# Kernel tuning notes

Hardware: AMD Instinct MI355X
Metric: run time of the kernel (lower is better)

Reference implementation:

```python
import jax, jax.numpy as jnp
import numpy as np

N_NODES = 100000
N_EDGES = 1600000
IN_DIM = 33
HID = 128
N_CLASSES = 10
N_GRAPHS = 128


def _glorot(key, shape):
    fan_in, fan_out = shape[0], shape[1]
    lim = (6.0 / (fan_in + fan_out)) ** 0.5
    return jax.random.uniform(key, shape, jnp.float32, -lim, lim)


def setup_inputs() -> dict:
    key = jax.random.key(0)
    ks = jax.random.split(key, 20)
    x = jax.random.normal(ks[0], (N_NODES, IN_DIM), jnp.float32)
    edge_index = jax.random.randint(ks[1], (2, N_EDGES), 0, N_NODES, jnp.int64)
    edge_w = jax.random.uniform(ks[2], (N_EDGES,), jnp.float32)
    batch = jnp.sort(jax.random.randint(ks[3], (N_NODES,), 0, N_GRAPHS, jnp.int64))
    p = {
        "We": _glorot(ks[4], (IN_DIM, HID)), "be": jnp.zeros((HID,), jnp.float32),
        "W1": _glorot(ks[5], (HID, HID)), "b1": jnp.zeros((HID,), jnp.float32),
        "W2": _glorot(ks[6], (HID, HID)), "b2": jnp.zeros((HID,), jnp.float32),
        "W3": _glorot(ks[7], (HID, HID)), "b3": jnp.zeros((HID,), jnp.float32),
        "W4": _glorot(ks[8], (HID, HID)), "b4": jnp.zeros((HID,), jnp.float32),
        "Wr1": _glorot(ks[9], (HID, HID // 2)), "br1": jnp.zeros((HID // 2,), jnp.float32),
        "Wr2": _glorot(ks[10], (HID // 2, HID // 4)), "br2": jnp.zeros((HID // 4,), jnp.float32),
        "Wr3": _glorot(ks[11], (HID // 4, N_CLASSES)),
    }
    return dict(x=x, edge_index=edge_index, edge_w=edge_w, batch=batch, **p)


def reference(x, edge_index, edge_w, batch,
              We, be, W1, b1, W2, b2, W3, b3, W4, b4,
              Wr1, br1, Wr2, br2, Wr3):
    N = x.shape[0]
    row, col = edge_index[0], edge_index[1]
    # PyG gcn_norm with add_self_loops=True: append (i,i) edges with weight 1
    loop = jnp.arange(N)
    row2 = jnp.concatenate([row, loop])
    col2 = jnp.concatenate([col, loop])
    w2 = jnp.concatenate([edge_w, jnp.ones((N,), edge_w.dtype)])
    deg = jax.ops.segment_sum(w2, col2, num_segments=N)  # in-degree incl. self-loop
    dinv = jnp.where(deg > 0, deg ** -0.5, 0.0)
    norm = dinv[row2] * w2 * dinv[col2]  # [E+N] symmetric normalization

    def conv(h, W, b):
        h = h @ W  # linear transform first (PyG GCNConv)
        msg = norm[:, None] * h[row2]  # gather + scale
        return jax.ops.segment_sum(msg, col2, num_segments=N) + b  # scatter-add to targets

    h = x @ We + be
    h = jax.nn.relu(conv(h, W1, b1))
    h = jax.nn.relu(conv(h, W2, b2))
    h = jax.nn.relu(conv(h, W3, b3))
    h = jax.nn.relu(conv(h, W4, b4))

    # global mean pool over graphs
    sums = jax.ops.segment_sum(h, batch, num_segments=N_GRAPHS)
    cnt = jax.ops.segment_sum(jnp.ones((N,), h.dtype), batch, num_segments=N_GRAPHS)
    pooled = sums / jnp.maximum(cnt, 1.0)[:, None]  # [G, HID]

    r = jax.nn.relu(pooled @ Wr1 + br1)
    r = jax.nn.relu(r @ Wr2 + br2)
    return r @ Wr3  # [G, n_classes]
```

## Files before the change

kernel.cpp:

```cpp
#include <hip/hip_runtime.h>
#include <hip/hip_bf16.h>

#define NN 100000
#define NE 1600000
#define IN_DIM 33
#define HID 128
#define NG 128
#define NCLS 10

using short8 = __attribute__((ext_vector_type(8))) short;
using floatx4 = __attribute__((ext_vector_type(4))) float;

static __device__ __forceinline__ size_t szmul(int a, int b) {
    return (size_t)a * (size_t)b;
}

static __device__ __forceinline__ unsigned short f2bf(float f) {
    unsigned u = __float_as_uint(f);
    u += 0x7fffu + ((u >> 16) & 1u);
    return (unsigned short)(u >> 16);
}
static __device__ __forceinline__ float bf_lo(unsigned u) { return __uint_as_float(u << 16); }
static __device__ __forceinline__ float bf_hi(unsigned u) { return __uint_as_float(u & 0xffff0000u); }

__global__ void k_init(int* bucket_cnt, int* bucket_fill, float* gsum) {
    int i = blockIdx.x * blockDim.x + threadIdx.x;
    if (i < 513) { bucket_cnt[i] = 0; bucket_fill[i] = 0; }
    if (i < NG * HID) gsum[i] = 0.0f;
}


__global__ __launch_bounds__(256) void k_bhist(const int* __restrict__ col,
                                               int* __restrict__ bucket_cnt, int e, int nbk) {
    __shared__ int hist[512];
    int tid = threadIdx.x;
    for (int i = tid; i < nbk; i += 256) hist[i] = 0;
    __syncthreads();
    for (int i = blockIdx.x * 256 + tid; i < e; i += 256 * 256)
        atomicAdd(&hist[col[i] >> 8], 1);
    __syncthreads();
    for (int i = tid; i < nbk; i += 256)
        if (hist[i]) atomicAdd(&bucket_cnt[i], hist[i]);
}

__global__ void k_scan_small(int* data, int nb) {
    __shared__ int s[512];
    int t = threadIdx.x;
    int v = (t < nb) ? data[t] : 0;
    s[t] = v;
    __syncthreads();
    for (int o = 1; o < 512; o <<= 1) {
        int a = (t >= o) ? s[t - o] : 0;
        __syncthreads();
        s[t] += a;
        __syncthreads();
    }
    if (t < nb) data[t] = s[t] - v;
    if (t == nb - 1) data[nb] = s[t];
}

__global__ __launch_bounds__(256) void k_bin_scatter(const int* __restrict__ row,
                                                     const int* __restrict__ col,
                                                     const float* __restrict__ w,
                                                     const int* __restrict__ bucket_base,
                                                     int* __restrict__ bucket_fill,
                                                     uint2* __restrict__ binned, int e, int nbk) {
    __shared__ int hist[512], rnk[512], basub[512];
    int tid = threadIdx.x;
    int c0 = blockIdx.x * 4096;
    for (int i = tid; i < nbk; i += 256) { hist[i] = 0; rnk[i] = 0; }
    __syncthreads();
    int myb[16]; unsigned myp[16]; unsigned myw[16];
#pragma unroll
    for (int u = 0; u < 16; ++u) {
        int idx = c0 + u * 256 + tid;
        int b = -1;
        if (idx < e) {
            int c = col[idx];
            int r = row[idx];
            myw[u] = __float_as_uint(w[idx]);
            b = c >> 8;
            myp[u] = ((unsigned)(c & 255) << 17) | (unsigned)r;
            atomicAdd(&hist[b], 1);
        }
        myb[u] = b;
    }
    __syncthreads();
    for (int i = tid; i < nbk; i += 256) {
        int c = hist[i];
        basub[i] = (c > 0) ? (bucket_base[i] + atomicAdd(&bucket_fill[i], c)) : 0;
    }
    __syncthreads();
#pragma unroll
    for (int u = 0; u < 16; ++u) {
        int b = myb[u];
        if (b >= 0) {
            int rk = atomicAdd(&rnk[b], 1);
            binned[basub[b] + rk] = make_uint2(myp[u], myw[u]);
        }
    }
}

__global__ __launch_bounds__(256) void k_bucket_cnt(const uint2* __restrict__ binned,
                                                    const int* __restrict__ bucket_base,
                                                    int* __restrict__ cnt,
                                                    float* __restrict__ wsum, int n) {
    __shared__ int c256[256];
    __shared__ float s256[256];
    int b = blockIdx.x, tid = threadIdx.x;
    c256[tid] = 0;
    s256[tid] = 0.0f;
    __syncthreads();
    int beg = bucket_base[b], end = bucket_base[b + 1];
    for (int e2 = beg + tid; e2 < end; e2 += 256) {
        uint2 rec = binned[e2];
        int lo = (rec.x >> 17) & 255;
        atomicAdd(&c256[lo], 1);
        atomicAdd(&s256[lo], __uint_as_float(rec.y));
    }
    __syncthreads();
    int node = b * 256 + tid;
    if (node < n) { cnt[node] = c256[tid]; wsum[node] = s256[tid]; }
}

__global__ void k_dinv(float* __restrict__ dinv, float* __restrict__ selfn, int n) {
    int i = blockIdx.x * blockDim.x + threadIdx.x;
    if (i >= n) return;
    float d = 1.0f + dinv[i];
    float di = (d > 0.0f) ? (1.0f / sqrtf(d)) : 0.0f;
    dinv[i] = di;
    selfn[i] = di * di;
}

#define SCAN_B 1024
__global__ void k_scan1(const int* __restrict__ cnt, int* __restrict__ rowptr,
                        int* __restrict__ bsums, int n) {
    __shared__ int s[SCAN_B];
    int t = threadIdx.x;
    int i = blockIdx.x * SCAN_B + t;
    int v = (i < n) ? cnt[i] : 0;
    s[t] = v;
    __syncthreads();
    for (int o = 1; o < SCAN_B; o <<= 1) {
        int a = (t >= o) ? s[t - o] : 0;
        __syncthreads();
        s[t] += a;
        __syncthreads();
    }
    if (i < n) rowptr[i] = s[t] - v;
    if (t == SCAN_B - 1) bsums[blockIdx.x] = s[t];
}

__global__ void k_scan3(int* rowptr, const int* __restrict__ bsums, int n, int etot) {
    int i = blockIdx.x * blockDim.x + threadIdx.x;
    if (i < n) rowptr[i] += bsums[i >> 10];
    else if (i == n) rowptr[n] = etot;
}

__global__ __launch_bounds__(256) void k_bucket_scatter(const uint2* __restrict__ binned,
                                                        const int* __restrict__ bucket_base,
                                                        const int* __restrict__ rowptr,
                                                        const float* __restrict__ dinv,
                                                        int2* __restrict__ csr, int n) {
    __shared__ int f256[256];
    int b = blockIdx.x, tid = threadIdx.x;
    f256[tid] = 0;
    __syncthreads();
    int beg = bucket_base[b], end = bucket_base[b + 1];
    for (int e2 = beg + tid; e2 < end; e2 += 256) {
        uint2 rec = binned[e2];
        int lo = (rec.x >> 17) & 255;
        int node = (b << 8) | lo;
        int src = rec.x & 0x1FFFF;
        float nw = dinv[src] * __uint_as_float(rec.y) * dinv[node];
        int pos = rowptr[node] + atomicAdd(&f256[lo], 1);
        csr[pos] = make_int2(src, __float_as_int(nw));
    }
    (void)n;
}

__global__ void k_combine(const float* __restrict__ We, const float* __restrict__ W1,
                          const float* __restrict__ be,
                          float* __restrict__ M, float* __restrict__ v) {
    int f = threadIdx.x;
    int k = blockIdx.x;
    if (k < IN_DIM) {
        float a = 0.0f;
#pragma unroll 8
        for (int j = 0; j < HID; ++j) a += We[k * HID + j] * W1[j * HID + f];
        M[k * HID + f] = a;
    } else {
        float a = 0.0f;
#pragma unroll 8
        for (int j = 0; j < HID; ++j) a += be[j] * W1[j * HID + f];
        v[f] = a;
    }
}

__global__ void k_wcast3(const float* __restrict__ W1, const float* __restrict__ W2,
                         const float* __restrict__ W3, unsigned short* __restrict__ Wt) {
    int k = blockIdx.x, c = threadIdx.x, l = blockIdx.y;
    const float* W = (l == 0) ? W1 : (l == 1) ? W2 : W3;
    Wt[((size_t)l * HID + c) * HID + k] = f2bf(W[k * HID + c]);
}

__global__ __launch_bounds__(256) void k_gemm_x(const float* __restrict__ x,
                                                const float* __restrict__ M,
                                                const float* __restrict__ v,
                                                unsigned short* __restrict__ tb, int n) {
    __shared__ float sX[32 * IN_DIM];
    int n0 = blockIdx.x * 32;
    int tid = threadIdx.x;
    int cnt = n - n0; if (cnt > 32) cnt = 32;
    for (int idx = tid; idx < cnt * IN_DIM; idx += 256)
        sX[idx] = x[szmul(n0, IN_DIM) + idx];
    __syncthreads();
    int f = tid & 127, g = tid >> 7;
    float Mc[IN_DIM];
#pragma unroll
    for (int k = 0; k < IN_DIM; ++k) Mc[k] = M[k * HID + f];
    float vf = v[f];
    int ndEnd = g * 16 + 16; if (ndEnd > cnt) ndEnd = cnt;
    for (int nd = g * 16; nd < ndEnd; ++nd) {
        float a = vf;
#pragma unroll
        for (int k = 0; k < IN_DIM; ++k) a += sX[nd * IN_DIM + k] * Mc[k];
        tb[szmul(n0 + nd, HID) + f] = f2bf(a);
    }
}

__global__ __launch_bounds__(256) void k_gemm_mfma(const unsigned short* __restrict__ A,
                                                   const unsigned short* __restrict__ Wt,
                                                   unsigned short* __restrict__ T, int n) {
    int wave = threadIdx.x >> 6;
    int lane = threadIdx.x & 63;
    int r = lane & 15, kg = lane >> 4;
    int row0 = blockIdx.x * 64 + wave * 16;
    int arow = row0 + r;
    short8 af[4];
#pragma unroll
    for (int kk = 0; kk < 4; ++kk) {
        if (arow < n)
            af[kk] = *reinterpret_cast<const short8*>(A + szmul(arow, HID) + kk * 32 + kg * 8);
        else
            af[kk] = short8{0, 0, 0, 0, 0, 0, 0, 0};
    }
    floatx4 acc[8];
#pragma unroll
    for (int ct = 0; ct < 8; ++ct) acc[ct] = floatx4{0.f, 0.f, 0.f, 0.f};
#pragma unroll
    for (int kk = 0; kk < 4; ++kk) {
#pragma unroll
        for (int ct = 0; ct < 8; ++ct) {
            short8 bf = *reinterpret_cast<const short8*>(
                Wt + (size_t)(ct * 16 + r) * HID + kk * 32 + kg * 8);
            acc[ct] = __builtin_amdgcn_mfma_f32_16x16x32_bf16(af[kk], bf, acc[ct], 0, 0, 0);
        }
    }
#pragma unroll
    for (int ct = 0; ct < 8; ++ct) {
#pragma unroll
        for (int reg = 0; reg < 4; ++reg) {
            int orow = row0 + kg * 4 + reg;
            if (orow < n)
                T[szmul(orow, HID) + ct * 16 + r] = f2bf(acc[ct][reg]);
        }
    }
}

__global__ __launch_bounds__(256) void k_aggregate(const uint4* __restrict__ tb,
                                                   const int* __restrict__ rowptr,
                                                   const int2* __restrict__ csr,
                                                   const float* __restrict__ selfn,
                                                   const float* __restrict__ bias,
                                                   uint4* __restrict__ hout, int n) {
    int i = (blockIdx.x * 256 + threadIdx.x) >> 4;
    if (i >= n) return;
    int p = threadIdx.x & 15;
    uint4 sv = tb[szmul(i, 16) + p];
    float sn = selfn[i];
    const float4* bp = reinterpret_cast<const float4*>(bias + p * 8);
    float4 b0 = bp[0], b1 = bp[1];
    float a0 = b0.x + sn * bf_lo(sv.x), a1 = b0.y + sn * bf_hi(sv.x);
    float a2 = b0.z + sn * bf_lo(sv.y), a3 = b0.w + sn * bf_hi(sv.y);
    float a4 = b1.x + sn * bf_lo(sv.z), a5 = b1.y + sn * bf_hi(sv.z);
    float a6 = b1.z + sn * bf_lo(sv.w), a7 = b1.w + sn * bf_hi(sv.w);
    int beg = rowptr[i], end = rowptr[i + 1];
#pragma unroll 4
    for (int j = beg; j < end; ++j) {
        int2 e = csr[j];
        float wj = __int_as_float(e.y);
        uint4 r = tb[szmul(e.x, 16) + p];
        a0 += wj * bf_lo(r.x); a1 += wj * bf_hi(r.x);
        a2 += wj * bf_lo(r.y); a3 += wj * bf_hi(r.y);
        a4 += wj * bf_lo(r.z); a5 += wj * bf_hi(r.z);
        a6 += wj * bf_lo(r.w); a7 += wj * bf_hi(r.w);
    }
    unsigned u0 = (unsigned)f2bf(fmaxf(a0, 0.f)) | ((unsigned)f2bf(fmaxf(a1, 0.f)) << 16);
    unsigned u1 = (unsigned)f2bf(fmaxf(a2, 0.f)) | ((unsigned)f2bf(fmaxf(a3, 0.f)) << 16);
    unsigned u2 = (unsigned)f2bf(fmaxf(a4, 0.f)) | ((unsigned)f2bf(fmaxf(a5, 0.f)) << 16);
    unsigned u3 = (unsigned)f2bf(fmaxf(a6, 0.f)) | ((unsigned)f2bf(fmaxf(a7, 0.f)) << 16);
    hout[szmul(i, 16) + p] = make_uint4(u0, u1, u2, u3);
}

__global__ void k_gcount_bs(const int* __restrict__ batch, int* gcnt, int n) {
    int g = threadIdx.x;
    if (g >= NG) return;
    int lo = 0, hi = n;
    while (lo < hi) { int mid = (lo + hi) >> 1; if (batch[mid] < g) lo = mid + 1; else hi = mid; }
    int start = lo;
    lo = 0; hi = n;
    while (lo < hi) { int mid = (lo + hi) >> 1; if (batch[mid] < g + 1) lo = mid + 1; else hi = mid; }
    gcnt[g] = lo - start;
}

__global__ __launch_bounds__(128) void k_pool(const unsigned short* __restrict__ h,
                                              const int* __restrict__ batch,
                                              float* gsum, int n) {
    int f = threadIdx.x;
    int i0 = blockIdx.x * 32;
    int i1 = min(i0 + 32, n);
    if (i0 >= n) return;
    float acc = 0.0f;
    int cur = batch[i0];
    for (int i = i0; i < i1; ++i) {
        int g = batch[i];
        if (g != cur) { atomicAdd(&gsum[cur * HID + f], acc); acc = 0.0f; cur = g; }
        acc += __uint_as_float((unsigned)h[szmul(i, HID) + f] << 16);
    }
    atomicAdd(&gsum[cur * HID + f], acc);
}

__global__ __launch_bounds__(128) void k_mlp(const float* __restrict__ gsum,
                                             const int* __restrict__ gcnt,
                                             const float* __restrict__ Wr1, const float* __restrict__ br1,
                                             const float* __restrict__ Wr2, const float* __restrict__ br2,
                                             const float* __restrict__ Wr3,
                                             float* __restrict__ out) {
    int g = blockIdx.x;
    int t = threadIdx.x;
    __shared__ float p[HID];
    __shared__ float r1[64];
    __shared__ float r2[32];
    float c = fmaxf((float)gcnt[g], 1.0f);
    p[t] = gsum[g * HID + t] / c;
    __syncthreads();
    if (t < 64) {
        float a = br1[t];
#pragma unroll 8
        for (int k = 0; k < HID; ++k) a += p[k] * Wr1[k * 64 + t];
        r1[t] = fmaxf(a, 0.0f);
    }
    __syncthreads();
    if (t < 32) {
        float a = br2[t];
#pragma unroll 8
        for (int k = 0; k < 64; ++k) a += r1[k] * Wr2[k * 32 + t];
        r2[t] = fmaxf(a, 0.0f);
    }
    __syncthreads();
    if (t < NCLS) {
        float a = 0.0f;
#pragma unroll
        for (int k = 0; k < 32; ++k) a += r2[k] * Wr3[k * NCLS + t];
        out[g * NCLS + t] = a;
    }
}

extern "C" void kernel_launch(void* const* d_in, const int* in_sizes, int n_in,
                              void* d_out, int out_size, void* d_ws, size_t ws_size,
                              hipStream_t stream) {
    const float* x     = (const float*)d_in[0];
    const int*   ei    = (const int*)d_in[1];
    const float* ew    = (const float*)d_in[2];
    const int*   batch = (const int*)d_in[3];
    const float* We  = (const float*)d_in[4];
    const float* be  = (const float*)d_in[5];
    const float* Wl[4] = { (const float*)d_in[6], (const float*)d_in[8],
                           (const float*)d_in[10], (const float*)d_in[12] };
    const float* bl[4] = { (const float*)d_in[7], (const float*)d_in[9],
                           (const float*)d_in[11], (const float*)d_in[13] };
    const float* Wr1 = (const float*)d_in[14];
    const float* br1 = (const float*)d_in[15];
    const float* Wr2 = (const float*)d_in[16];
    const float* br2 = (const float*)d_in[17];
    const float* Wr3 = (const float*)d_in[18];
    float* out = (float*)d_out;

    const int N = in_sizes[3];
    const int E = in_sizes[2];
    const int* row = ei;
    const int* col = ei + E;
    const int nbk = (N + 255) >> 8;

    char* w = (char*)d_ws;
    size_t off = 0;
    auto alloc = [&](size_t bytes) -> void* {
        void* p = w + off;
        off = (off + bytes + 255) & ~(size_t)255;
        return p;
    };
    float* dinv       = (float*)alloc((size_t)N * 4);
    float* selfn      = (float*)alloc((size_t)N * 4);
    int*   cnt        = (int*)  alloc((size_t)N * 4);
    int*   rowptr     = (int*)  alloc((size_t)(N + 1) * 4);
    int*   bsums      = (int*)  alloc(4096);
    int*   bucket_cnt = (int*)  alloc(513 * 4);
    int*   bucket_fill= (int*)  alloc(513 * 4);
    int2*  csr        = (int2*) alloc((size_t)E * 8);
    unsigned short* h  = (unsigned short*)alloc((size_t)N * HID * 2);
    unsigned short* tb = (unsigned short*)alloc((size_t)N * HID * 2);
    unsigned short* Wt = (unsigned short*)alloc((size_t)3 * HID * HID * 2);
    float* M          = (float*)alloc((size_t)IN_DIM * HID * 4);
    float* vbe        = (float*)alloc((size_t)HID * 4);
    float* gsum       = (float*)alloc((size_t)NG * HID * 4);
    int*   gcnt       = (int*)  alloc((size_t)NG * 4);
    uint2* binned     = (uint2*)tb;
    (void)ws_size;

    auto cdiv = [](int a, int b) { return (a + b - 1) / b; };

    k_init<<<64, 256, 0, stream>>>(bucket_cnt, bucket_fill, gsum);
    k_bhist<<<256, 256, 0, stream>>>(col, bucket_cnt, E, nbk);
    k_scan_small<<<1, 512, 0, stream>>>(bucket_cnt, nbk);
    k_bin_scatter<<<cdiv(E, 4096), 256, 0, stream>>>(row, col, ew, bucket_cnt,
                                                     bucket_fill, binned, E, nbk);
    k_bucket_cnt<<<nbk, 256, 0, stream>>>(binned, bucket_cnt, cnt, dinv, N);
    k_dinv<<<cdiv(N, 256), 256, 0, stream>>>(dinv, selfn, N);

    int nb = cdiv(N, SCAN_B);
    k_scan1<<<nb, SCAN_B, 0, stream>>>(cnt, rowptr, bsums, N);
    k_scan_small<<<1, 512, 0, stream>>>(bsums, nb);
    k_scan3<<<cdiv(N + 1, 256), 256, 0, stream>>>(rowptr, bsums, N, E);
    k_bucket_scatter<<<nbk, 256, 0, stream>>>(binned, bucket_cnt, rowptr, dinv, csr, N);

    k_combine<<<IN_DIM + 1, HID, 0, stream>>>(We, Wl[0], be, M, vbe);
    k_wcast3<<<dim3(HID, 3), HID, 0, stream>>>(Wl[1], Wl[2], Wl[3], Wt);

    k_gemm_x<<<cdiv(N, 32), 256, 0, stream>>>(x, M, vbe, tb, N);
    k_aggregate<<<cdiv(N, 16), 256, 0, stream>>>((const uint4*)tb, rowptr, csr,
                                                 selfn, bl[0], (uint4*)h, N);

    for (int l = 1; l < 4; ++l) {
        k_gemm_mfma<<<cdiv(N, 64), 256, 0, stream>>>(h, Wt + (size_t)(l - 1) * HID * HID,
                                                     tb, N);
        k_aggregate<<<cdiv(N, 16), 256, 0, stream>>>((const uint4*)tb, rowptr, csr,
                                                     selfn, bl[l], (uint4*)h, N);
    }

    k_gcount_bs<<<1, 128, 0, stream>>>(batch, gcnt, N);
    k_pool<<<cdiv(N, 32), 128, 0, stream>>>(h, batch, gsum, N);
    k_mlp<<<NG, HID, 0, stream>>>(gsum, gcnt, Wr1, br1, Wr2, br2, Wr3, out);

    (void)out_size; (void)n_in;
}
```

Baseline: 500.7 us.

## Vectorize edge binning, fuse rowptr scan into bucket pass, widen MFMA GEMM tile

Edge binning now loads col/row/weights as contiguous int4/float4 per thread instead of strided scalars. The rowptr computation is moved into the per-bucket count kernel: a local 256-wide scan is added to the bucket base offset, which removes the three-kernel global scan and the cnt/bsums buffers. The MFMA GEMM now processes 32 rows per wave with two accumulator sets to reuse weight loads, and writes packed bf16 pairs via a lane shuffle. This uses more registers per wave, and the changed edge-to-thread mapping alters the order of the shared-memory atomics.

```diff
diff --git a/kernel.cpp b/kernel.cpp
--- a/kernel.cpp
+++ b/kernel.cpp
@@ -70,20 +70,41 @@
     int c0 = blockIdx.x * 4096;
     for (int i = tid; i < nbk; i += 256) { hist[i] = 0; rnk[i] = 0; }
     __syncthreads();
+    int base = c0 + tid * 16;
     int myb[16]; unsigned myp[16]; unsigned myw[16];
-#pragma unroll
-    for (int u = 0; u < 16; ++u) {
-        int idx = c0 + u * 256 + tid;
-        int b = -1;
-        if (idx < e) {
-            int c = col[idx];
-            int r = row[idx];
-            myw[u] = __float_as_uint(w[idx]);
-            b = c >> 8;
-            myp[u] = ((unsigned)(c & 255) << 17) | (unsigned)r;
-            atomicAdd(&hist[b], 1);
+    if (base + 16 <= e) {
+#pragma unroll
+        for (int q = 0; q < 4; ++q) {
+            int4 c4 = reinterpret_cast<const int4*>(col + base)[q];
+            int4 r4 = reinterpret_cast<const int4*>(row + base)[q];
+            float4 w4 = reinterpret_cast<const float4*>(w + base)[q];
+            int cs[4] = {c4.x, c4.y, c4.z, c4.w};
+            int rs[4] = {r4.x, r4.y, r4.z, r4.w};
+            float ws[4] = {w4.x, w4.y, w4.z, w4.w};
+#pragma unroll
+            for (int v = 0; v < 4; ++v) {
+                int c = cs[v];
+                int b = c >> 8;
+                myb[q * 4 + v] = b;
+                myp[q * 4 + v] = ((unsigned)(c & 255) << 17) | (unsigned)rs[v];
+                myw[q * 4 + v] = __float_as_uint(ws[v]);
+                atomicAdd(&hist[b], 1);
+            }
         }
-        myb[u] = b;
+    } else {
+#pragma unroll
+        for (int v = 0; v < 16; ++v) {
+            int idx = base + v;
+            int b = -1;
+            if (idx < e) {
+                int c = col[idx];
+                myw[v] = __float_as_uint(w[idx]);
+                b = c >> 8;
+                myp[v] = ((unsigned)(c & 255) << 17) | (unsigned)row[idx];
+                atomicAdd(&hist[b], 1);
+            }
+            myb[v] = b;
+        }
     }
     __syncthreads();
     for (int i = tid; i < nbk; i += 256) {
@@ -101,12 +122,13 @@
     }
 }
 
-__global__ __launch_bounds__(256) void k_bucket_cnt(const uint2* __restrict__ binned,
-                                                    const int* __restrict__ bucket_base,
-                                                    int* __restrict__ cnt,
-                                                    float* __restrict__ wsum, int n) {
+__global__ __launch_bounds__(256) void k_bucket_rowptr(const uint2* __restrict__ binned,
+                                                       const int* __restrict__ bucket_base,
+                                                       int* __restrict__ rowptr,
+                                                       float* __restrict__ wsum, int n) {
     __shared__ int c256[256];
     __shared__ float s256[256];
+    __shared__ int sc[256];
     int b = blockIdx.x, tid = threadIdx.x;
     c256[tid] = 0;
     s256[tid] = 0.0f;
@@ -119,42 +141,31 @@
         atomicAdd(&s256[lo], __uint_as_float(rec.y));
     }
     __syncthreads();
+    int v = c256[tid];
+    sc[tid] = v;
+    __syncthreads();
+    for (int o = 1; o < 256; o <<= 1) {
+        int a = (tid >= o) ? sc[tid - o] : 0;
+        __syncthreads();
+        sc[tid] += a;
+        __syncthreads();
+    }
     int node = b * 256 + tid;
-    if (node < n) { cnt[node] = c256[tid]; wsum[node] = s256[tid]; }
-}
-
-__global__ void k_dinv(float* __restrict__ dinv, float* __restrict__ selfn, int n) {
+    if (node < n) {
+        rowptr[node] = beg + sc[tid] - v;
+        wsum[node] = s256[tid];
+    }
+}
+
+__global__ void k_dinv(float* __restrict__ dinv, float* __restrict__ selfn,
+                       int* __restrict__ rowptr, int n, int etot) {
     int i = blockIdx.x * blockDim.x + threadIdx.x;
+    if (i == n) rowptr[n] = etot;
     if (i >= n) return;
     float d = 1.0f + dinv[i];
     float di = (d > 0.0f) ? (1.0f / sqrtf(d)) : 0.0f;
     dinv[i] = di;
     selfn[i] = di * di;
-}
-
-#define SCAN_B 1024
-__global__ void k_scan1(const int* __restrict__ cnt, int* __restrict__ rowptr,
-                        int* __restrict__ bsums, int n) {
-    __shared__ int s[SCAN_B];
-    int t = threadIdx.x;
-    int i = blockIdx.x * SCAN_B + t;
-    int v = (i < n) ? cnt[i] : 0;
-    s[t] = v;
-    __syncthreads();
-    for (int o = 1; o < SCAN_B; o <<= 1) {
-        int a = (t >= o) ? s[t - o] : 0;
-        __syncthreads();
-        s[t] += a;
-        __syncthreads();
-    }
-    if (i < n) rowptr[i] = s[t] - v;
-    if (t == SCAN_B - 1) bsums[blockIdx.x] = s[t];
-}
-
-__global__ void k_scan3(int* rowptr, const int* __restrict__ bsums, int n, int etot) {
-    int i = blockIdx.x * blockDim.x + threadIdx.x;
-    if (i < n) rowptr[i] += bsums[i >> 10];
-    else if (i == n) rowptr[n] = etot;
 }
 
 __global__ __launch_bounds__(256) void k_bucket_scatter(const uint2* __restrict__ binned,
@@ -235,35 +246,49 @@
     int wave = threadIdx.x >> 6;
     int lane = threadIdx.x & 63;
     int r = lane & 15, kg = lane >> 4;
-    int row0 = blockIdx.x * 64 + wave * 16;
-    int arow = row0 + r;
-    short8 af[4];
+    int row0 = blockIdx.x * 128 + wave * 32;
+    short8 af0[4], af1[4];
 #pragma unroll
     for (int kk = 0; kk < 4; ++kk) {
-        if (arow < n)
-            af[kk] = *reinterpret_cast<const short8*>(A + szmul(arow, HID) + kk * 32 + kg * 8);
-        else
-            af[kk] = short8{0, 0, 0, 0, 0, 0, 0, 0};
-    }
-    floatx4 acc[8];
-#pragma unroll
-    for (int ct = 0; ct < 8; ++ct) acc[ct] = floatx4{0.f, 0.f, 0.f, 0.f};
+        int a0 = row0 + r, a1 = row0 + 16 + r;
+        af0[kk] = (a0 < n) ? *reinterpret_cast<const short8*>(A + szmul(a0, HID) + kk * 32 + kg * 8)
+                           : short8{0, 0, 0, 0, 0, 0, 0, 0};
+        af1[kk] = (a1 < n) ? *reinterpret_cast<const short8*>(A + szmul(a1, HID) + kk * 32 + kg * 8)
+                           : short8{0, 0, 0, 0, 0, 0, 0, 0};
+    }
+    floatx4 acc0[8], acc1[8];
+#pragma unroll
+    for (int ct = 0; ct < 8; ++ct) {
+        acc0[ct] = floatx4{0.f, 0.f, 0.f, 0.f};
+        acc1[ct] = floatx4{0.f, 0.f, 0.f, 0.f};
+    }
 #pragma unroll
     for (int kk = 0; kk < 4; ++kk) {
 #pragma unroll
         for (int ct = 0; ct < 8; ++ct) {
             short8 bf = *reinterpret_cast<const short8*>(
                 Wt + (size_t)(ct * 16 + r) * HID + kk * 32 + kg * 8);
-            acc[ct] = __builtin_amdgcn_mfma_f32_16x16x32_bf16(af[kk], bf, acc[ct], 0, 0, 0);
+            acc0[ct] = __builtin_amdgcn_mfma_f32_16x16x32_bf16(af0[kk], bf, acc0[ct], 0, 0, 0);
+            acc1[ct] = __builtin_amdgcn_mfma_f32_16x16x32_bf16(af1[kk], bf, acc1[ct], 0, 0, 0);
         }
     }
+    bool even = (r & 1) == 0;
 #pragma unroll
     for (int ct = 0; ct < 8; ++ct) {
 #pragma unroll
         for (int reg = 0; reg < 4; ++reg) {
-            int orow = row0 + kg * 4 + reg;
-            if (orow < n)
-                T[szmul(orow, HID) + ct * 16 + r] = f2bf(acc[ct][reg]);
+            float o0 = __shfl_xor(acc0[ct][reg], 1);
+            float o1 = __shfl_xor(acc1[ct][reg], 1);
+            int orow0 = row0 + kg * 4 + reg;
+            int orow1 = orow0 + 16;
+            if (even && orow0 < n) {
+                unsigned pk = (unsigned)f2bf(acc0[ct][reg]) | ((unsigned)f2bf(o0) << 16);
+                *reinterpret_cast<unsigned*>(T + szmul(orow0, HID) + ct * 16 + r) = pk;
+            }
+            if (even && orow1 < n) {
+                unsigned pk = (unsigned)f2bf(acc1[ct][reg]) | ((unsigned)f2bf(o1) << 16);
+                *reinterpret_cast<unsigned*>(T + szmul(orow1, HID) + ct * 16 + r) = pk;
+            }
         }
     }
 }
@@ -402,9 +427,7 @@
     };
     float* dinv       = (float*)alloc((size_t)N * 4);
     float* selfn      = (float*)alloc((size_t)N * 4);
-    int*   cnt        = (int*)  alloc((size_t)N * 4);
     int*   rowptr     = (int*)  alloc((size_t)(N + 1) * 4);
-    int*   bsums      = (int*)  alloc(4096);
     int*   bucket_cnt = (int*)  alloc(513 * 4);
     int*   bucket_fill= (int*)  alloc(513 * 4);
     int2*  csr        = (int2*) alloc((size_t)E * 8);
@@ -425,13 +448,8 @@
     k_scan_small<<<1, 512, 0, stream>>>(bucket_cnt, nbk);
     k_bin_scatter<<<cdiv(E, 4096), 256, 0, stream>>>(row, col, ew, bucket_cnt,
                                                      bucket_fill, binned, E, nbk);
-    k_bucket_cnt<<<nbk, 256, 0, stream>>>(binned, bucket_cnt, cnt, dinv, N);
-    k_dinv<<<cdiv(N, 256), 256, 0, stream>>>(dinv, selfn, N);
-
-    int nb = cdiv(N, SCAN_B);
-    k_scan1<<<nb, SCAN_B, 0, stream>>>(cnt, rowptr, bsums, N);
-    k_scan_small<<<1, 512, 0, stream>>>(bsums, nb);
-    k_scan3<<<cdiv(N + 1, 256), 256, 0, stream>>>(rowptr, bsums, N, E);
+    k_bucket_rowptr<<<nbk, 256, 0, stream>>>(binned, bucket_cnt, rowptr, dinv, N);
+    k_dinv<<<cdiv(N + 1, 256), 256, 0, stream>>>(dinv, selfn, rowptr, N, E);
     k_bucket_scatter<<<nbk, 256, 0, stream>>>(binned, bucket_cnt, rowptr, dinv, csr, N);
 
     k_combine<<<IN_DIM + 1, HID, 0, stream>>>(We, Wl[0], be, M, vbe);
@@ -442,8 +460,8 @@
                                                  selfn, bl[0], (uint4*)h, N);
 
     for (int l = 1; l < 4; ++l) {
-        k_gemm_mfma<<<cdiv(N, 64), 256, 0, stream>>>(h, Wt + (size_t)(l - 1) * HID * HID,
-                                                     tb, N);
+        k_gemm_mfma<<<cdiv(N, 128), 256, 0, stream>>>(h, Wt + (size_t)(l - 1) * HID * HID,
+                                                      tb, N);
         k_aggregate<<<cdiv(N, 16), 256, 0, stream>>>((const uint4*)tb, rowptr, csr,
                                                      selfn, bl[l], (uint4*)h, N);
     }
```

New measurement: 470.1 us. 1.07x faster.
